# Kernel optimization log

Measured on AMD Instinct MI355X. Metric: run time of the kernel, lower is better.

The kernel has to match this reference:

```python
import jax, jax.numpy as jnp
import numpy as np

SIGMA = 1.0


def setup_inputs() -> dict:
    key = jax.random.key(0)
    k1, k2, k3 = jax.random.split(key, 3)
    B, N = 32, 1024
    y_pred = jax.random.normal(k1, (B, N), dtype=jnp.float32)
    y_true = jax.random.normal(k2, (B, N), dtype=jnp.float32)
    masks = jax.random.randint(k3, (B, N), 0, 2, dtype=jnp.int32)
    return {"y_pred": y_pred, "y_true": y_true, "masks": masks}


def _lambda_ndcg(y_pred, y_true, masks, sigma=SIGMA):
    # masks: [B, N] int; valid where > 0
    m = (masks > 0)
    mf = m.astype(y_pred.dtype)                      # [B, N]
    # Position of each valid item within the compressed valid list (0-indexed k).
    # Torch code: discount[k] = 1 / log2(k + 2). cumsum gives k+1, so log2(cumsum+1).
    cs = jnp.cumsum(mf, axis=1)                      # [B, N], 1-indexed count at valid slots
    disc = jnp.where(m, 1.0 / jnp.log2(cs + 1.0), 0.0)  # [B, N]

    pred_diff = y_pred[:, :, None] - y_pred[:, None, :]   # [B, N, N]
    true_diff = y_true[:, :, None] - y_true[:, None, :]   # [B, N, N]
    pair_valid = mf[:, :, None] * mf[:, None, :]          # both items valid
    pos_mask = (true_diff > 0).astype(y_pred.dtype) * pair_valid
    pairwise_weight = disc[:, :, None] + disc[:, None, :]
    # log1p(exp(-sigma * d)) == softplus(-sigma * d), numerically stable
    pair_loss = jax.nn.softplus(-sigma * pred_diff) * pos_mask * pairwise_weight

    per_row = pair_loss.sum(axis=(1, 2)) / (pos_mask.sum(axis=(1, 2)) + 1e-12)  # [B]
    # Rows with < 2 valid items have zero positive pairs -> contribute 0, matching
    # the torch `continue`; divisor is always batch_size.
    return per_row.sum() / y_pred.shape[0]


def reference(y_pred, y_true, masks):
    return _lambda_ndcg(y_pred, y_true, masks)
```

## Files before the change

kernel.cpp:

```cpp
#include <hip/hip_runtime.h>
#include <math.h>

#define Bq 32
#define Nq 1024
#define BPR 16
#define TPB 256


__global__ __launch_bounds__(1024)
void prep_kernel(const float* __restrict__ yp,
                 const float* __restrict__ yt,
                 const int* __restrict__ masks,
                 float4* __restrict__ cw,
                 float* __restrict__ acc,
                 int* __restrict__ vcount,
                 int* __restrict__ done) {
    const int row = blockIdx.x;
    const int t = threadIdx.x;
    const int lane = t & 63;
    const int wid = t >> 6;

    const int mv = (masks[row * Nq + t] > 0) ? 1 : 0;

    int val = mv;
#pragma unroll
    for (int off = 1; off < 64; off <<= 1) {
        int n = __shfl_up(val, off, 64);
        if (lane >= off) val += n;
    }

    __shared__ int wsum[16];
    if (lane == 63) wsum[wid] = val;
    __syncthreads();

    if (wid == 0 && lane < 16) {
        int v = wsum[lane];
#pragma unroll
        for (int off = 1; off < 16; off <<= 1) {
            int n = __shfl_up(v, off, 16);
            if (lane >= off) v += n;
        }
        wsum[lane] = v;
    }
    __syncthreads();

    const int cs = val + (wid > 0 ? wsum[wid - 1] : 0);
    const int V = wsum[15];

    if (mv) {
        const float d = 1.0f / log2f((float)cs + 1.0f);
        cw[row * Nq + (cs - 1)] = make_float4(yp[row * Nq + t], yt[row * Nq + t], d, 0.0f);
    }
    if (t == 0) {
        vcount[row] = V;
        acc[2 * row + 0] = 0.0f;
        acc[2 * row + 1] = 0.0f;
    }
    if (row == 0 && t == 1) *done = 0;
}

__global__ __launch_bounds__(TPB)
void pair_kernel(const float4* __restrict__ cw,
                 float* __restrict__ acc,
                 const int* __restrict__ vcount,
                 int* __restrict__ done,
                 float* __restrict__ out) {
    const int row = blockIdx.y;
    const int V = vcount[row];

    __shared__ float4 sv[Nq];
    for (int s = threadIdx.x; s < V; s += TPB) sv[s] = cw[row * Nq + s];
    __syncthreads();

    const int P = V * (V - 1) / 2;
    const int T = BPR * TPB;
    const int tgl = blockIdx.x * TPB + threadIdx.x;
    const int chunk = (P + T - 1) / T;
    const int k0 = tgl * chunk;
    const int k1 = min(k0 + chunk, P);

    float loss = 0.0f;
    float cnt = 0.0f;

    if (k0 < k1) {
        int i = (int)((1.0 + sqrt(1.0 + 8.0 * (double)k0)) * 0.5);
        if (i < 1) i = 1;
        while (i * (i - 1) / 2 > k0) --i;
        while ((i + 1) * i / 2 <= k0) ++i;
        int j = k0 - i * (i - 1) / 2;

        float4 qi = sv[i];
#pragma unroll 1
        for (int k = k0; k < k1; ++k) {
            const float4 qj = sv[j];
            const bool win = qi.y > qj.y;
            const float x = win ? (qj.x - qi.x) : (qi.x - qj.x);
            const float a = __expf(-fabsf(x));
            const float spv = fmaxf(x, 0.0f) + __logf(1.0f + a);
            const bool ok = (qi.y != qj.y);
            const float w = ok ? (qi.z + qj.z) : 0.0f;
            loss = fmaf(spv, w, loss);
            cnt += ok ? 1.0f : 0.0f;
            if (++j == i) { j = 0; ++i; if (i < V) qi = sv[i]; }
        }
    }

    const int lane = threadIdx.x & 63;
    const int wid = threadIdx.x >> 6;
#pragma unroll
    for (int off = 32; off > 0; off >>= 1) {
        loss += __shfl_down(loss, off, 64);
        cnt  += __shfl_down(cnt, off, 64);
    }
    __shared__ float rl[4], rc[4];
    if (lane == 0) { rl[wid] = loss; rc[wid] = cnt; }
    __syncthreads();

    if (threadIdx.x == 0) {
        const float L = rl[0] + rl[1] + rl[2] + rl[3];
        const float C = rc[0] + rc[1] + rc[2] + rc[3];
        atomicAdd(&acc[2 * row + 0], L);
        atomicAdd(&acc[2 * row + 1], C);
        __threadfence();
        const int old = __hip_atomic_fetch_add(done, 1, __ATOMIC_ACQ_REL, __HIP_MEMORY_SCOPE_AGENT);
        if (old == BPR * Bq - 1) {
            float s = 0.0f;
            for (int r = 0; r < Bq; ++r) {
                const float L2 = __hip_atomic_load(&acc[2 * r + 0], __ATOMIC_RELAXED, __HIP_MEMORY_SCOPE_AGENT);
                const float C2 = __hip_atomic_load(&acc[2 * r + 1], __ATOMIC_RELAXED, __HIP_MEMORY_SCOPE_AGENT);
                s += L2 / (C2 + 1e-12f);
            }
            out[0] = s / (float)Bq;
        }
    }
}

extern "C" void kernel_launch(void* const* d_in, const int* in_sizes, int n_in,
                              void* d_out, int out_size, void* d_ws, size_t ws_size,
                              hipStream_t stream) {
    const float* y_pred = (const float*)d_in[0];
    const float* y_true = (const float*)d_in[1];
    const int*   masks  = (const int*)d_in[2];
    float* out = (float*)d_out;

    float4* cw    = (float4*)d_ws;
    float*  acc   = (float*)(cw + Bq * Nq);
    int*    vcount= (int*)(acc + 2 * Bq);
    int*    done  = vcount + Bq;

    prep_kernel<<<Bq, 1024, 0, stream>>>(y_pred, y_true, masks, cw, acc, vcount, done);
    pair_kernel<<<dim3(BPR, Bq), TPB, 0, stream>>>(cw, acc, vcount, done, out);
}
```

Measured before the change: 81.30 us.

## Fuse prefix-scan prep into pair kernel, compacting valid items directly in LDS

Removes the separate prep kernel and its global compacted buffer. Each pair-kernel block now redoes the mask prefix scan for its row, with 4 elements per thread, and writes the compacted (pred, true, discount) tuples straight into shared memory. Accumulator and counter zeroing move to a hipMemsetAsync. This cuts one kernel launch and a global round trip, at the cost of each of the 16 blocks per row repeating the scan.

```diff
diff --git a/kernel.cpp b/kernel.cpp
--- a/kernel.cpp
+++ b/kernel.cpp
@@ -5,76 +5,63 @@
 #define Nq 1024
 #define BPR 16
 #define TPB 256
+#define NBLK (BPR * Bq)
 
 
-__global__ __launch_bounds__(1024)
-void prep_kernel(const float* __restrict__ yp,
-                 const float* __restrict__ yt,
-                 const int* __restrict__ masks,
-                 float4* __restrict__ cw,
-                 float* __restrict__ acc,
-                 int* __restrict__ vcount,
-                 int* __restrict__ done) {
-    const int row = blockIdx.x;
-    const int t = threadIdx.x;
-    const int lane = t & 63;
-    const int wid = t >> 6;
+__global__ __launch_bounds__(TPB)
+void fused_kernel(const float* __restrict__ yp,
+                  const float* __restrict__ yt,
+                  const int* __restrict__ masks,
+                  float* __restrict__ acc,
+                  int* __restrict__ done,
+                  float* __restrict__ out) {
+    const int row = blockIdx.y;
+    const int tid = threadIdx.x;
+    const int lane = tid & 63;
+    const int wid = tid >> 6;
 
-    const int mv = (masks[row * Nq + t] > 0) ? 1 : 0;
+    __shared__ float4 sv[Nq];
+    __shared__ int wsum[4];
+    __shared__ float rl[4], rc[4];
 
-    int val = mv;
+    const int b0 = tid * 4;
+    int m0 = masks[row * Nq + b0 + 0] > 0;
+    int m1 = masks[row * Nq + b0 + 1] > 0;
+    int m2 = masks[row * Nq + b0 + 2] > 0;
+    int m3 = masks[row * Nq + b0 + 3] > 0;
+    const int tot = m0 + m1 + m2 + m3;
+
+    int val = tot;
 #pragma unroll
     for (int off = 1; off < 64; off <<= 1) {
         int n = __shfl_up(val, off, 64);
         if (lane >= off) val += n;
     }
-
-    __shared__ int wsum[16];
     if (lane == 63) wsum[wid] = val;
     __syncthreads();
 
-    if (wid == 0 && lane < 16) {
-        int v = wsum[lane];
+    int wbase = 0;
 #pragma unroll
-        for (int off = 1; off < 16; off <<= 1) {
-            int n = __shfl_up(v, off, 16);
-            if (lane >= off) v += n;
+    for (int w = 0; w < 4; ++w) wbase += (w < wid) ? wsum[w] : 0;
+    const int V = wsum[0] + wsum[1] + wsum[2] + wsum[3];
+    int rank = wbase + val - tot;
+
+    {
+        int mm[4] = {m0, m1, m2, m3};
+#pragma unroll
+        for (int k = 0; k < 4; ++k) {
+            if (mm[k]) {
+                const float d = 1.0f / log2f((float)rank + 2.0f);
+                sv[rank] = make_float4(yp[row * Nq + b0 + k], yt[row * Nq + b0 + k], d, 0.0f);
+                ++rank;
+            }
         }
-        wsum[lane] = v;
     }
     __syncthreads();
 
-    const int cs = val + (wid > 0 ? wsum[wid - 1] : 0);
-    const int V = wsum[15];
-
-    if (mv) {
-        const float d = 1.0f / log2f((float)cs + 1.0f);
-        cw[row * Nq + (cs - 1)] = make_float4(yp[row * Nq + t], yt[row * Nq + t], d, 0.0f);
-    }
-    if (t == 0) {
-        vcount[row] = V;
-        acc[2 * row + 0] = 0.0f;
-        acc[2 * row + 1] = 0.0f;
-    }
-    if (row == 0 && t == 1) *done = 0;
-}
-
-__global__ __launch_bounds__(TPB)
-void pair_kernel(const float4* __restrict__ cw,
-                 float* __restrict__ acc,
-                 const int* __restrict__ vcount,
-                 int* __restrict__ done,
-                 float* __restrict__ out) {
-    const int row = blockIdx.y;
-    const int V = vcount[row];
-
-    __shared__ float4 sv[Nq];
-    for (int s = threadIdx.x; s < V; s += TPB) sv[s] = cw[row * Nq + s];
-    __syncthreads();
-
     const int P = V * (V - 1) / 2;
-    const int T = BPR * TPB;
-    const int tgl = blockIdx.x * TPB + threadIdx.x;
+    const int T = NBLK / Bq * TPB;
+    const int tgl = blockIdx.x * TPB + tid;
     const int chunk = (P + T - 1) / T;
     const int k0 = tgl * chunk;
     const int k1 = min(k0 + chunk, P);
@@ -105,25 +92,22 @@
         }
     }
 
-    const int lane = threadIdx.x & 63;
-    const int wid = threadIdx.x >> 6;
 #pragma unroll
     for (int off = 32; off > 0; off >>= 1) {
         loss += __shfl_down(loss, off, 64);
         cnt  += __shfl_down(cnt, off, 64);
     }
-    __shared__ float rl[4], rc[4];
     if (lane == 0) { rl[wid] = loss; rc[wid] = cnt; }
     __syncthreads();
 
-    if (threadIdx.x == 0) {
+    if (tid == 0) {
         const float L = rl[0] + rl[1] + rl[2] + rl[3];
         const float C = rc[0] + rc[1] + rc[2] + rc[3];
         atomicAdd(&acc[2 * row + 0], L);
         atomicAdd(&acc[2 * row + 1], C);
         __threadfence();
         const int old = __hip_atomic_fetch_add(done, 1, __ATOMIC_ACQ_REL, __HIP_MEMORY_SCOPE_AGENT);
-        if (old == BPR * Bq - 1) {
+        if (old == NBLK - 1) {
             float s = 0.0f;
             for (int r = 0; r < Bq; ++r) {
                 const float L2 = __hip_atomic_load(&acc[2 * r + 0], __ATOMIC_RELAXED, __HIP_MEMORY_SCOPE_AGENT);
@@ -143,11 +127,9 @@
     const int*   masks  = (const int*)d_in[2];
     float* out = (float*)d_out;
 
-    float4* cw    = (float4*)d_ws;
-    float*  acc   = (float*)(cw + Bq * Nq);
-    int*    vcount= (int*)(acc + 2 * Bq);
-    int*    done  = vcount + Bq;
+    float* acc  = (float*)d_ws;
+    int*   done = (int*)(acc + 2 * Bq);
 
-    prep_kernel<<<Bq, 1024, 0, stream>>>(y_pred, y_true, masks, cw, acc, vcount, done);
-    pair_kernel<<<dim3(BPR, Bq), TPB, 0, stream>>>(cw, acc, vcount, done, out);
+    hipMemsetAsync(d_ws, 0, 2 * Bq * sizeof(float) + sizeof(int), stream);
+    fused_kernel<<<dim3(BPR, Bq), TPB, 0, stream>>>(y_pred, y_true, masks, acc, done, out);
 }
```

New measurement: 81.68 us. No clear change (+0.5%).
